# Kernel optimization log

Measured on AMD Instinct MI355X. Metric: run time of the kernel, lower is better.

## Reference

```python
import jax, jax.numpy as jnp
import numpy as np

V_IN = 32000
V_OUT = 32000
E = 1024
H = 1024
B = 16
T = 512


def _lstm_layer(xs, Wih, Whh, bih, bhh):
    # xs: [T, B, in_dim]; PyTorch gate order: i, f, g, o (each size H)
    gx = jnp.einsum('tbi,gi->tbg', xs, Wih) + bih + bhh  # [T, B, 4H]

    def step(carry, g_t):
        h, c = carry
        g = g_t + h @ Whh.T  # [B, 4H]
        i, f, gg, o = jnp.split(g, 4, axis=-1)
        i = jax.nn.sigmoid(i)
        f = jax.nn.sigmoid(f)
        gg = jnp.tanh(gg)
        o = jax.nn.sigmoid(o)
        c = f * c + i * gg
        h = o * jnp.tanh(c)
        return (h, c), h

    h0 = jnp.zeros((xs.shape[1], Whh.shape[1]), dtype=xs.dtype)
    c0 = jnp.zeros_like(h0)
    _, hs = jax.lax.scan(step, (h0, c0), gx)
    return hs  # [T, B, H]


def setup_inputs() -> dict:
    key = jax.random.key(0)
    ks = jax.random.split(key, 12)
    s_e = 1.0  # nn.Embedding default init is N(0,1)
    s_l = 1.0 / np.sqrt(H)  # LSTM/Linear uniform bound 1/sqrt(H)

    def u(k, shape):
        return jax.random.uniform(k, shape, jnp.float32, -s_l, s_l)

    return {
        'x': jax.random.randint(ks[0], (B, T), 0, V_IN),
        'emb': jax.random.normal(ks[1], (V_IN, E), jnp.float32) * s_e,
        'W_ih0': u(ks[2], (4 * H, E)),
        'W_hh0': u(ks[3], (4 * H, H)),
        'b_ih0': u(ks[4], (4 * H,)),
        'b_hh0': u(ks[5], (4 * H,)),
        'W_ih1': u(ks[6], (4 * H, H)),
        'W_hh1': u(ks[7], (4 * H, H)),
        'b_ih1': u(ks[8], (4 * H,)),
        'b_hh1': u(ks[9], (4 * H,)),
        'W_out': u(ks[10], (V_OUT, H)),
        'b_out': u(ks[11], (V_OUT,)),
    }


def reference(x, emb, W_ih0, W_hh0, b_ih0, b_hh0, W_ih1, W_hh1, b_ih1, b_hh1, W_out, b_out):
    # embedding + permute to [T, B, E]
    out = emb[x].transpose(1, 0, 2)
    out = _lstm_layer(out, W_ih0, W_hh0, b_ih0, b_hh0)
    out = _lstm_layer(out, W_ih1, W_hh1, b_ih1, b_hh1)
    logits = jnp.einsum('tbh,oh->tbo', out, W_out) + b_out
    return logits.transpose(1, 0, 2)  # [B, T, V_OUT]
```

## Files before the change

kernel.cpp:

```cpp
#include <hip/hip_runtime.h>
#include <cstdint>
#include <cstddef>

typedef __bf16 bf16;
typedef float f32x4 __attribute__((ext_vector_type(4)));
typedef bf16 bf16x8 __attribute__((ext_vector_type(8)));
typedef bf16 bf16x4 __attribute__((ext_vector_type(4)));

#define AS1 __attribute__((address_space(1)))
#define AS3 __attribute__((address_space(3)))

__device__ __forceinline__ void gload_lds16(const void* g, void* l) {
  __builtin_amdgcn_global_load_lds((AS1 void*)g, (AS3 void*)l, 16, 0, 0);
}

#define RING 8
#define FLAG_WORDS 1024

__global__ __launch_bounds__(256) void init_misc(
    const float* __restrict__ bih0, const float* __restrict__ bhh0,
    const float* __restrict__ bih1, const float* __restrict__ bhh1,
    float* __restrict__ bsum0, float* __restrict__ bsum1, unsigned* __restrict__ flags) {
  int i = blockIdx.x * 256 + threadIdx.x;
  if (i < 4096) {
    bsum0[i] = bih0[i] + bhh0[i];
    bsum1[i] = bih1[i] + bhh1[i];
  }
  if (i < FLAG_WORDS) flags[i] = 0u;
}

__global__ __launch_bounds__(256) void embed_gather(
    const int* __restrict__ x, const float* __restrict__ emb, bf16* __restrict__ xe, int T) {
  int row = blockIdx.x;
  int t = row >> 4, b = row & 15;
  int tok = x[b * T + t];
  int cix = threadIdx.x << 2;
  f32x4 v = *(const f32x4*)(emb + ((size_t)tok << 10) + cix);
  bf16x4 o;
  for (int j = 0; j < 4; ++j) o[j] = (bf16)v[j];
  *(bf16x4*)(xe + ((size_t)row << 10) + cix) = o;
}

template <int OUTMODE>
__global__ __launch_bounds__(256) void gemm_bf16(
    const bf16* __restrict__ A, const float* __restrict__ Bw,
    const float* __restrict__ bias, float* __restrict__ C,
    int M, int N, int K, int Tdim) {
  __shared__ bf16 aL[2][128 * 32];
  __shared__ bf16 bL[2][128 * 32];
  const int tid = threadIdx.x;
  const int l = tid & 63, w = tid >> 6;
  const int nbm = M >> 7;
  const int bm = blockIdx.x % nbm;
  const int bn = blockIdx.x / nbm;
  const int wr = (w >> 1) << 6, wc = (w & 1) << 6;
  const int NT = K >> 5;
  const int r16 = l & 15, kq = l >> 4;

  f32x4 acc[4][4];
  for (int m = 0; m < 4; ++m)
    for (int n = 0; n < 4; ++n) acc[m][n] = (f32x4){0.f, 0.f, 0.f, 0.f};

  for (int i = 0; i < 2; ++i) {
    int lin = tid + (i << 8);
    int r = lin >> 2, s = lin & 3, c = s ^ (r & 3);
    gload_lds16(A + (size_t)((bm << 7) + r) * K + (c << 3), &aL[0][lin << 3]);
  }
  for (int i = 0; i < 2; ++i) {
    int lin = tid + (i << 8);
    int r = lin >> 2, c = lin & 3;
    const float* src = Bw + (size_t)((bn << 7) + r) * K + (c << 3);
    f32x4 v0 = *(const f32x4*)src;
    f32x4 v1 = *(const f32x4*)(src + 4);
    bf16x8 o;
    for (int j = 0; j < 4; ++j) { o[j] = (bf16)v0[j]; o[j + 4] = (bf16)v1[j]; }
    *(bf16x8*)&bL[0][(r << 5) + ((c ^ (r & 3)) << 3)] = o;
  }
  __syncthreads();

  for (int kt = 0; kt < NT; ++kt) {
    const int cur = kt & 1;
    const bool pf = (kt + 1 < NT);
    f32x4 bv0[2], bv1[2];
    int br_[2], bs_[2];
    if (pf) {
      for (int i = 0; i < 2; ++i) {
        int lin = tid + (i << 8);
        int r = lin >> 2, s = lin & 3, c = s ^ (r & 3);
        gload_lds16(A + (size_t)((bm << 7) + r) * K + ((kt + 1) << 5) + (c << 3),
                    &aL[cur ^ 1][lin << 3]);
      }
      for (int i = 0; i < 2; ++i) {
        int lin = tid + (i << 8);
        int r = lin >> 2, c = lin & 3;
        const float* src = Bw + (size_t)((bn << 7) + r) * K + ((kt + 1) << 5) + (c << 3);
        bv0[i] = *(const f32x4*)src;
        bv1[i] = *(const f32x4*)(src + 4);
        br_[i] = r;
        bs_[i] = c ^ (r & 3);
      }
    }
    bf16x8 af[4], bfr[4];
    for (int m = 0; m < 4; ++m) {
      int row = wr + (m << 4) + r16;
      int ch = kq ^ (row & 3);
      af[m] = *(const bf16x8*)&aL[cur][(row << 5) + (ch << 3)];
    }
    for (int n = 0; n < 4; ++n) {
      int row = wc + (n << 4) + r16;
      int ch = kq ^ (row & 3);
      bfr[n] = *(const bf16x8*)&bL[cur][(row << 5) + (ch << 3)];
    }
    for (int m = 0; m < 4; ++m)
      for (int n = 0; n < 4; ++n)
        acc[m][n] = __builtin_amdgcn_mfma_f32_16x16x32_bf16(af[m], bfr[n], acc[m][n], 0, 0, 0);
    if (pf) {
      for (int i = 0; i < 2; ++i) {
        bf16x8 o;
        for (int j = 0; j < 4; ++j) { o[j] = (bf16)bv0[i][j]; o[j + 4] = (bf16)bv1[i][j]; }
        *(bf16x8*)&bL[cur ^ 1][(br_[i] << 5) + (bs_[i] << 3)] = o;
      }
    }
    __syncthreads();
  }

  float bvv[4];
  for (int n = 0; n < 4; ++n) bvv[n] = bias[(bn << 7) + wc + (n << 4) + r16];
  for (int m = 0; m < 4; ++m) {
    int Rbase = (bm << 7) + wr + (m << 4) + (kq << 2);
    for (int r = 0; r < 4; ++r) {
      int R = Rbase + r;
      size_t rowoff;
      if (OUTMODE == 0) {
        rowoff = (size_t)R * N;
      } else {
        int tt = R >> 4, bb = R & 15;
        rowoff = ((size_t)bb * Tdim + tt) * N;
      }
      for (int n = 0; n < 4; ++n)
        C[rowoff + (bn << 7) + wc + (n << 4) + r16] = acc[m][n][r] + bvv[n];
    }
  }
}

__global__ __launch_bounds__(256, 1) void lstm_pipe3(
    const float* __restrict__ gx,
    const float* __restrict__ Whh0,
    const float* __restrict__ Wih1,
    const float* __restrict__ Whh1,
    const float* __restrict__ bsum1,
    bf16* __restrict__ hs0t,
    bf16* __restrict__ hs1t,
    float* __restrict__ gx1,
    bf16* __restrict__ hs1rm,
    unsigned* __restrict__ flags,
    int T) {
  __shared__ bf16 wlds[4][16 * 1024];
  __shared__ unsigned short hb[4][64];
  __shared__ unsigned tokv[4];
  const int tid = threadIdx.x;
  const int l = tid & 63, w = tid >> 6;
  const int bid = blockIdx.x;
  const int r16 = l & 15, kq = l >> 4;
  unsigned* const fL0 = flags;
  unsigned* const fB = flags + 256;
  unsigned* const fL1 = flags + 512;
  const int typ = bid >> 6;
  const int lb = bid & 63;
  const int widx = lb * 4 + w;
  const int colbase = lb * 16 + w * 4;

  {
    const float* Wsrc = (typ == 0) ? Whh0 : ((typ == 1) ? Wih1 : Whh1);
    for (int it = 0; it < 32; ++it) {
      int lin = it * 64 + l;
      int row = lin >> 7, cs = lin & 127, c = cs ^ (row & 7);
      const float* s = Wsrc + (size_t)((row >> 2) * 1024 + colbase + (row & 3)) * 1024 + c * 8;
      f32x4 v0 = *(const f32x4*)s;
      f32x4 v1 = *(const f32x4*)(s + 4);
      bf16x8 o;
      for (int j = 0; j < 4; ++j) { o[j] = (bf16)v0[j]; o[j + 4] = (bf16)v1[j]; }
      *(bf16x8*)&wlds[w][row * 1024 + cs * 8] = o;
    }
  }
  if (tid < 4) tokv[tid] = 0;
  __syncthreads();

  const int gcol = (r16 >> 2) * 1024 + colbase + (r16 & 3);
  const int b0s = (r16 >> 2) & 1, b1s = (r16 >> 3) & 1;

  auto pollq = [&](unsigned* arr, unsigned tgt) {
    unsigned* q = arr + w * 64 + (l & 15) * 4;
    for (;;) {
      unsigned a0 = __hip_atomic_load(q + 0, __ATOMIC_RELAXED, __HIP_MEMORY_SCOPE_AGENT);
      unsigned a1 = __hip_atomic_load(q + 1, __ATOMIC_RELAXED, __HIP_MEMORY_SCOPE_AGENT);
      unsigned a2 = __hip_atomic_load(q + 2, __ATOMIC_RELAXED, __HIP_MEMORY_SCOPE_AGENT);
      unsigned a3 = __hip_atomic_load(q + 3, __ATOMIC_RELAXED, __HIP_MEMORY_SCOPE_AGENT);
      if (__all(a0 >= tgt && a1 >= tgt && a2 >= tgt && a3 >= tgt)) break;
      __builtin_amdgcn_s_sleep(2);
    }
    volatile unsigned* tk = tokv;
    if (l == 0) tk[w] = tgt;
    while (tk[0] < tgt || tk[1] < tgt || tk[2] < tgt || tk[3] < tgt) {
    }
    asm volatile("" ::: "memory");
  };
  auto poll1 = [&](unsigned* p, unsigned tgt) {
    while (__hip_atomic_load(p, __ATOMIC_RELAXED, __HIP_MEMORY_SCOPE_AGENT) < tgt)
      __builtin_amdgcn_s_sleep(2);
    asm volatile("" ::: "memory");
  };
  auto chain = [&](const bf16* plane) -> f32x4 {
    f32x4 acc = (f32x4){0.f, 0.f, 0.f, 0.f};
    const char* hp = (const char*)plane;
#pragma unroll 8
    for (int kk = 0; kk < 32; ++kk) {
      int tl = kk * 8 + kq * 2;
      unsigned long long lo = *(const unsigned long long*)(hp + tl * 128 + r16 * 8);
      unsigned long long hi = *(const unsigned long long*)(hp + tl * 128 + 128 + r16 * 8);
      union { struct { unsigned long long a, b; } u; bf16x8 v; } A;
      A.u.a = lo;
      A.u.b = hi;
      bf16x8 Bf = *(const bf16x8*)&wlds[w][r16 * 1024 + (((kk * 4 + kq) ^ (r16 & 7)) << 3)];
      acc = __builtin_amdgcn_mfma_f32_16x16x32_bf16(A.v, Bf, acc, 0, 0, 0);
    }
    return acc;
  };

  if (typ == 1) {
    const float bsv = bsum1[gcol];
    unsigned* const myflag = fB + widx;
    unsigned* const partner = fL1 + widx;
    for (int t = 0; t < T; ++t) {
      if (t >= RING) poll1(partner, (unsigned)(t - RING + 1));
      pollq(fL0, (unsigned)(t + 1));
      f32x4 acc = chain(hs0t + (size_t)t * 16384);
      for (int r = 0; r < 4; ++r) acc[r] += bsv;
      float* dst = gx1 + (size_t)(t & (RING - 1)) * 65536 + widx * 256 + r16 * 16 + kq * 4;
      asm volatile("global_store_dwordx4 %0, %1, off sc0 sc1" ::"v"(dst), "v"(acc) : "memory");
      asm volatile("s_waitcnt vmcnt(0)" ::: "memory");
      if (l == 0)
        __hip_atomic_store(myflag, (unsigned)(t + 1), __ATOMIC_RELAXED, __HIP_MEMORY_SCOPE_AGENT);
    }
    return;
  }

  float cst[4] = {0.f, 0.f, 0.f, 0.f};
  unsigned* const myflag = (typ == 0) ? (fL0 + widx) : (fL1 + widx);
  unsigned* const bpartner = fB + widx;
  bf16* const houts = (typ == 0) ? hs0t : hs1t;

  for (int t = 0; t < T; ++t) {
    float gxv[4];
    if (typ == 0) {
      for (int r = 0; r < 4; ++r)
        gxv[r] = gx[(size_t)(t * 16 + kq * 4 + r) * 4096 + gcol];
    }
    if (typ == 0) {
      if (t > 0) pollq(fL0, (unsigned)t);
    } else {
      poll1(bpartner, (unsigned)(t + 1));
      if (t > 0) pollq(fL1, (unsigned)t);
    }
    f32x4 acc = (f32x4){0.f, 0.f, 0.f, 0.f};
    if (t > 0) acc = chain(houts + (size_t)(t - 1) * 16384);
    if (typ == 0) {
      for (int r = 0; r < 4; ++r) acc[r] += gxv[r];
    } else {
      const float* gp = gx1 + (size_t)(t & (RING - 1)) * 65536 + widx * 256 + r16 * 16 + kq * 4;
      f32x4 g1;
      asm volatile("global_load_dwordx4 %0, %1, off sc0 sc1\ns_waitcnt vmcnt(0)"
                   : "=v"(g1) : "v"(gp) : "memory");
      for (int r = 0; r < 4; ++r) acc[r] += g1[r];
    }
    float hv[4];
    for (int r = 0; r < 4; ++r) {
      float own = acc[r];
      float p4 = __shfl_xor(own, 4, 64);
      float ev = b0s ? p4 : own;
      float ov = b0s ? own : p4;
      float ev8 = __shfl_xor(ev, 8, 64);
      float ov8 = __shfl_xor(ov, 8, 64);
      float xi = b1s ? ev8 : ev;
      float xf = b1s ? ov8 : ov;
      float xg = b1s ? ev : ev8;
      float xo = b1s ? ov : ov8;
      float ig = 1.f / (1.f + __expf(-xi));
      float fg = 1.f / (1.f + __expf(-xf));
      float eg = __expf(2.f * xg);
      float gv = 1.f - 2.f / (eg + 1.f);
      float og = 1.f / (1.f + __expf(-xo));
      cst[r] = fg * cst[r] + ig * gv;
      float ec = __expf(2.f * cst[r]);
      float th = 1.f - 2.f / (ec + 1.f);
      hv[r] = og * th;
    }
    if (r16 < 4) {
      volatile unsigned short* hbp = hb[w];
      for (int r = 0; r < 4; ++r) {
        bf16 hbv = (bf16)hv[r];
        hbp[(kq * 4 + r) * 4 + r16] = __builtin_bit_cast(unsigned short, hbv);
      }
    }
    unsigned long long rowv = 0;
    if (l < 16) rowv = *(volatile unsigned long long*)&hb[w][l * 4];
    if (l < 16) {
      char* dst = (char*)houts + (size_t)t * 32768 + widx * 128 + l * 8;
      asm volatile("global_store_dwordx2 %0, %1, off sc0 sc1" ::"v"(dst), "v"(rowv) : "memory");
    }
    asm volatile("s_waitcnt vmcnt(0)" ::: "memory");
    if (l == 0)
      __hip_atomic_store(myflag, (unsigned)(t + 1), __ATOMIC_RELAXED, __HIP_MEMORY_SCOPE_AGENT);
    if (typ == 1 + 1 && l < 16) {
      *(unsigned long long*)((char*)hs1rm + ((size_t)(t * 16 + l) * 1024 + colbase) * 2) = rowv;
    }
  }
}

extern "C" void kernel_launch(void* const* d_in, const int* in_sizes, int n_in,
                              void* d_out, int out_size, void* d_ws, size_t ws_size,
                              hipStream_t stream) {
  const int* x = (const int*)d_in[0];
  const float* emb = (const float*)d_in[1];
  const float* Wih0 = (const float*)d_in[2];
  const float* Whh0 = (const float*)d_in[3];
  const float* bih0 = (const float*)d_in[4];
  const float* bhh0 = (const float*)d_in[5];
  const float* Wih1 = (const float*)d_in[6];
  const float* Whh1 = (const float*)d_in[7];
  const float* bih1 = (const float*)d_in[8];
  const float* bhh1 = (const float*)d_in[9];
  const float* Wout = (const float*)d_in[10];
  const float* bout = (const float*)d_in[11];

  const int T = 512, H = 1024, V = 32000;
  const int M = T * 16;
  const size_t bfb = (size_t)M * H * 2;
  const size_t out_bytes = (size_t)out_size * 4;

  char* p = (char*)d_ws;
  bf16* hs1rm = (bf16*)p;         p += bfb;
  float* bsum0 = (float*)p;       p += 4096 * 4;
  float* bsum1 = (float*)p;       p += 4096 * 4;
  unsigned* flags = (unsigned*)p; p += FLAG_WORDS * 4;

  float* gx = (float*)d_out;
  float* gx1 = (float*)((char*)d_out + (512ull << 20));
  char* tail = (char*)d_out + out_bytes - 3 * bfb;
  bf16* xe = (bf16*)tail;
  bf16* hs0t = (bf16*)(tail + bfb);
  bf16* hs1t = (bf16*)(tail + 2 * bfb);

  init_misc<<<64, 256, 0, stream>>>(bih0, bhh0, bih1, bhh1, bsum0, bsum1, flags);
  embed_gather<<<M, 256, 0, stream>>>(x, emb, xe, T);
  gemm_bf16<0><<<(M / 128) * (4096 / 128), 256, 0, stream>>>(xe, Wih0, bsum0, gx, M, 4096, H, 0);
  lstm_pipe3<<<192, 256, 0, stream>>>(gx, Whh0, Wih1, Whh1, bsum1, hs0t, hs1t, gx1, hs1rm,
                                      flags, T);
  gemm_bf16<1><<<(M / 128) * (V / 128), 256, 0, stream>>>(hs1rm, Wout, bout, (float*)d_out,
                                                          M, V, H, T);
}
```

Baseline: 5.294 ms.

## Overlap output projection with LSTM recurrence in one persistent kernel

Merges the recurrent LSTM pipeline and the vocabulary projection GEMM into a single persistent kernel. It launches 64 extra blocks, and once the recurrent blocks finish they also pull output tiles from an atomic work queue, gated on per-row-chunk progress flags. This lets the large output GEMM run while the sequential recurrence is still going. The embedding gather is fused into the input-projection GEMM, and gx/hs/gx1 scratch buffers are placed inside not-yet-written regions of the output tensor in a new layout. The cost is more complex synchronization, and there is a risk that the scratch aliases get overwritten by output tiles before the recurrence has finished reading them.

Result: slower. 5.912 ms (+11.7%).

```diff
diff --git a/kernel.cpp b/kernel.cpp
--- a/kernel.cpp
+++ b/kernel.cpp
@@ -5,7 +5,6 @@
 typedef __bf16 bf16;
 typedef float f32x4 __attribute__((ext_vector_type(4)));
 typedef bf16 bf16x8 __attribute__((ext_vector_type(8)));
-typedef bf16 bf16x4 __attribute__((ext_vector_type(4)));
 
 #define AS1 __attribute__((address_space(1)))
 #define AS3 __attribute__((address_space(3)))
@@ -14,8 +13,13 @@
   __builtin_amdgcn_global_load_lds((AS1 void*)g, (AS3 void*)l, 16, 0, 0);
 }
 
-#define RING 8
 #define FLAG_WORDS 1024
+#define NTILE 16000u
+#define RW 32000ull
+
+__device__ __forceinline__ size_t LROW(int b, int t) {
+  return ((size_t)b * 512 + (size_t)t) * RW;
+}
 
 __global__ __launch_bounds__(256) void init_misc(
     const float* __restrict__ bih0, const float* __restrict__ bhh0,
@@ -29,77 +33,48 @@
   if (i < FLAG_WORDS) flags[i] = 0u;
 }
 
-__global__ __launch_bounds__(256) void embed_gather(
-    const int* __restrict__ x, const float* __restrict__ emb, bf16* __restrict__ xe, int T) {
-  int row = blockIdx.x;
-  int t = row >> 4, b = row & 15;
-  int tok = x[b * T + t];
-  int cix = threadIdx.x << 2;
-  f32x4 v = *(const f32x4*)(emb + ((size_t)tok << 10) + cix);
-  bf16x4 o;
-  for (int j = 0; j < 4; ++j) o[j] = (bf16)v[j];
-  *(bf16x4*)(xe + ((size_t)row << 10) + cix) = o;
-}
-
-template <int OUTMODE>
-__global__ __launch_bounds__(256) void gemm_bf16(
-    const bf16* __restrict__ A, const float* __restrict__ Bw,
-    const float* __restrict__ bias, float* __restrict__ C,
-    int M, int N, int K, int Tdim) {
-  __shared__ bf16 aL[2][128 * 32];
-  __shared__ bf16 bL[2][128 * 32];
+__global__ __launch_bounds__(256) void gemm_emb(
+    const int* __restrict__ x, const float* __restrict__ emb,
+    const float* __restrict__ Wih0, const float* __restrict__ bsum0,
+    float* __restrict__ C) {
+  __shared__ bf16 aL[2][4096];
+  __shared__ bf16 bL[2][4096];
   const int tid = threadIdx.x;
   const int l = tid & 63, w = tid >> 6;
-  const int nbm = M >> 7;
-  const int bm = blockIdx.x % nbm;
-  const int bn = blockIdx.x / nbm;
+  const int bm = blockIdx.x & 63;
+  const int bn = blockIdx.x >> 6;
   const int wr = (w >> 1) << 6, wc = (w & 1) << 6;
-  const int NT = K >> 5;
   const int r16 = l & 15, kq = l >> 4;
 
   f32x4 acc[4][4];
   for (int m = 0; m < 4; ++m)
     for (int n = 0; n < 4; ++n) acc[m][n] = (f32x4){0.f, 0.f, 0.f, 0.f};
 
-  for (int i = 0; i < 2; ++i) {
-    int lin = tid + (i << 8);
-    int r = lin >> 2, s = lin & 3, c = s ^ (r & 3);
-    gload_lds16(A + (size_t)((bm << 7) + r) * K + (c << 3), &aL[0][lin << 3]);
-  }
-  for (int i = 0; i < 2; ++i) {
-    int lin = tid + (i << 8);
-    int r = lin >> 2, c = lin & 3;
-    const float* src = Bw + (size_t)((bn << 7) + r) * K + (c << 3);
-    f32x4 v0 = *(const f32x4*)src;
-    f32x4 v1 = *(const f32x4*)(src + 4);
-    bf16x8 o;
-    for (int j = 0; j < 4; ++j) { o[j] = (bf16)v0[j]; o[j + 4] = (bf16)v1[j]; }
-    *(bf16x8*)&bL[0][(r << 5) + ((c ^ (r & 3)) << 3)] = o;
-  }
+  auto stage = [&](int kt, int buf) {
+    for (int i = 0; i < 2; ++i) {
+      int lin = tid + (i << 8);
+      int r = lin >> 2, c = lin & 3;
+      int rg = (bm << 7) + r;
+      int tok = x[((rg & 15) << 9) + (rg >> 4)];
+      const float* sa = emb + ((size_t)tok << 10) + (kt << 5) + (c << 3);
+      f32x4 a0 = *(const f32x4*)sa;
+      f32x4 a1 = *(const f32x4*)(sa + 4);
+      bf16x8 oa;
+      for (int j = 0; j < 4; ++j) { oa[j] = (bf16)a0[j]; oa[j + 4] = (bf16)a1[j]; }
+      *(bf16x8*)&aL[buf][(r << 5) + ((c ^ (r & 3)) << 3)] = oa;
+      const float* sb = Wih0 + (size_t)((bn << 7) + r) * 1024 + (kt << 5) + (c << 3);
+      f32x4 b0 = *(const f32x4*)sb;
+      f32x4 b1 = *(const f32x4*)(sb + 4);
+      bf16x8 ob;
+      for (int j = 0; j < 4; ++j) { ob[j] = (bf16)b0[j]; ob[j + 4] = (bf16)b1[j]; }
+      *(bf16x8*)&bL[buf][(r << 5) + ((c ^ (r & 3)) << 3)] = ob;
+    }
+  };
+  stage(0, 0);
   __syncthreads();
-
-  for (int kt = 0; kt < NT; ++kt) {
-    const int cur = kt & 1;
-    const bool pf = (kt + 1 < NT);
-    f32x4 bv0[2], bv1[2];
-    int br_[2], bs_[2];
-    if (pf) {
-      for (int i = 0; i < 2; ++i) {
-        int lin = tid + (i << 8);
-        int r = lin >> 2, s = lin & 3, c = s ^ (r & 3);
-        gload_lds16(A + (size_t)((bm << 7) + r) * K + ((kt + 1) << 5) + (c << 3),
-                    &aL[cur ^ 1][lin << 3]);
-      }
-      for (int i = 0; i < 2; ++i) {
-        int lin = tid + (i << 8);
-        int r = lin >> 2, c = lin & 3;
-        const float* src = Bw + (size_t)((bn << 7) + r) * K + ((kt + 1) << 5) + (c << 3);
-        bv0[i] = *(const f32x4*)src;
-        bv1[i] = *(const f32x4*)(src + 4);
-        br_[i] = r;
-        bs_[i] = c ^ (r & 3);
-      }
-    }
+  for (int kt = 0; kt < 32; ++kt) {
+    int cur = kt & 1;
+    if (kt + 1 < 32) stage(kt + 1, cur ^ 1);
     bf16x8 af[4], bfr[4];
     for (int m = 0; m < 4; ++m) {
       int row = wr + (m << 4) + r16;
@@ -114,63 +89,46 @@
     for (int m = 0; m < 4; ++m)
       for (int n = 0; n < 4; ++n)
         acc[m][n] = __builtin_amdgcn_mfma_f32_16x16x32_bf16(af[m], bfr[n], acc[m][n], 0, 0, 0);
-    if (pf) {
-      for (int i = 0; i < 2; ++i) {
-        bf16x8 o;
-        for (int j = 0; j < 4; ++j) { o[j] = (bf16)bv0[i][j]; o[j + 4] = (bf16)bv1[i][j]; }
-        *(bf16x8*)&bL[cur ^ 1][(br_[i] << 5) + (bs_[i] << 3)] = o;
-      }
-    }
     __syncthreads();
   }
-
   float bvv[4];
-  for (int n = 0; n < 4; ++n) bvv[n] = bias[(bn << 7) + wc + (n << 4) + r16];
+  for (int n = 0; n < 4; ++n) bvv[n] = bsum0[(bn << 7) + wc + (n << 4) + r16];
   for (int m = 0; m < 4; ++m) {
     int Rbase = (bm << 7) + wr + (m << 4) + (kq << 2);
     for (int r = 0; r < 4; ++r) {
       int R = Rbase + r;
-      size_t rowoff;
-      if (OUTMODE == 0) {
-        rowoff = (size_t)R * N;
-      } else {
-        int tt = R >> 4, bb = R & 15;
-        rowoff = ((size_t)bb * Tdim + tt) * N;
-      }
+      int tt = R >> 4, bb = R & 15;
+      size_t rowoff = LROW(bb, tt);
       for (int n = 0; n < 4; ++n)
         C[rowoff + (bn << 7) + wc + (n << 4) + r16] = acc[m][n][r] + bvv[n];
     }
   }
 }
 
-__global__ __launch_bounds__(256, 1) void lstm_pipe3(
-    const float* __restrict__ gx,
-    const float* __restrict__ Whh0,
-    const float* __restrict__ Wih1,
-    const float* __restrict__ Whh1,
-    const float* __restrict__ bsum1,
-    bf16* __restrict__ hs0t,
-    bf16* __restrict__ hs1t,
-    float* __restrict__ gx1,
-    bf16* __restrict__ hs1rm,
-    unsigned* __restrict__ flags,
-    int T) {
+__global__ __launch_bounds__(256, 1) void lstm_mega(
+    const float* __restrict__ Whh0, const float* __restrict__ Wih1,
+    const float* __restrict__ Whh1, const float* __restrict__ bsum1,
+    bf16* __restrict__ hs1rm, const float* __restrict__ Wout,
+    const float* __restrict__ bout, float* __restrict__ C,
+    unsigned* __restrict__ flags) {
   __shared__ bf16 wlds[4][16 * 1024];
   __shared__ unsigned short hb[4][64];
-  __shared__ unsigned tokv[4];
-  const int tid = threadIdx.x;
-  const int l = tid & 63, w = tid >> 6;
+  __shared__ unsigned tokv[3][4];
+  __shared__ unsigned qsh;
+  const int tid = threadIdx.x, l = tid & 63, w = tid >> 6;
   const int bid = blockIdx.x;
   const int r16 = l & 15, kq = l >> 4;
   unsigned* const fL0 = flags;
   unsigned* const fB = flags + 256;
   unsigned* const fL1 = flags + 512;
+  unsigned* const qctr = flags + 768;
   const int typ = bid >> 6;
   const int lb = bid & 63;
   const int widx = lb * 4 + w;
   const int colbase = lb * 16 + w * 4;
-
-  {
+  const int T = 512;
+
+  if (typ < 3) {
     const float* Wsrc = (typ == 0) ? Whh0 : ((typ == 1) ? Wih1 : Whh1);
     for (int it = 0; it < 32; ++it) {
       int lin = it * 64 + l;
@@ -183,13 +141,10 @@
       *(bf16x8*)&wlds[w][row * 1024 + cs * 8] = o;
     }
   }
-  if (tid < 4) tokv[tid] = 0;
+  if (tid < 12) ((unsigned*)tokv)[tid] = 0;
   __syncthreads();
 
-  const int gcol = (r16 >> 2) * 1024 + colbase + (r16 & 3);
-  const int b0s = (r16 >> 2) & 1, b1s = (r16 >> 3) & 1;
-
-  auto pollq = [&](unsigned* arr, unsigned tgt) {
+  auto pollq = [&](int gid, unsigned* arr, unsigned tgt) {
     unsigned* q = arr + w * 64 + (l & 15) * 4;
     for (;;) {
       unsigned a0 = __hip_atomic_load(q + 0, __ATOMIC_RELAXED, __HIP_MEMORY_SCOPE_AGENT);
@@ -199,8 +154,8 @@
       if (__all(a0 >= tgt && a1 >= tgt && a2 >= tgt && a3 >= tgt)) break;
       __builtin_amdgcn_s_sleep(2);
     }
-    volatile unsigned* tk = tokv;
-    if (l == 0) tk[w] = tgt;
+    volatile unsigned* tk = tokv[gid];
+    if (l == 0 && tk[w] < tgt) tk[w] = tgt;
     while (tk[0] < tgt || tk[1] < tgt || tk[2] < tgt || tk[3] < tgt) {
     }
     asm volatile("" ::: "memory");
@@ -226,54 +181,17 @@
     }
     return acc;
   };
-
-  if (typ == 1) {
-    const float bsv = bsum1[gcol];
-    unsigned* const myflag = fB + widx;
-    unsigned* const partner = fL1 + widx;
-    for (int t = 0; t < T; ++t) {
-      if (t >= RING) poll1(partner, (unsigned)(t - RING + 1));
-      pollq(fL0, (unsigned)(t + 1));
-      f32x4 acc = chain(hs0t + (size_t)t * 16384);
-      for (int r = 0; r < 4; ++r) acc[r] += bsv;
-      float* dst = gx1 + (size_t)(t & (RING - 1)) * 65536 + widx * 256 + r16 * 16 + kq * 4;
-      asm volatile("global_store_dwordx4 %0, %1, off sc0 sc1" ::"v"(dst), "v"(acc) : "memory");
-      asm volatile("s_waitcnt vmcnt(0)" ::: "memory");
-      if (l == 0)
-        __hip_atomic_store(myflag, (unsigned)(t + 1), __ATOMIC_RELAXED, __HIP_MEMORY_SCOPE_AGENT);
-    }
-    return;
-  }
-
-  float cst[4] = {0.f, 0.f, 0.f, 0.f};
-  unsigned* const myflag = (typ == 0) ? (fL0 + widx) : (fL1 + widx);
-  unsigned* const bpartner = fB + widx;
-  bf16* const houts = (typ == 0) ? hs0t : hs1t;
-
-  for (int t = 0; t < T; ++t) {
-    float gxv[4];
-    if (typ == 0) {
-      for (int r = 0; r < 4; ++r)
-        gxv[r] = gx[(size_t)(t * 16 + kq * 4 + r) * 4096 + gcol];
-    }
-    if (typ == 0) {
-      if (t > 0) pollq(fL0, (unsigned)t);
-    } else {
-      poll1(bpartner, (unsigned)(t + 1));
-      if (t > 0) pollq(fL1, (unsigned)t);
-    }
-    f32x4 acc = (f32x4){0.f, 0.f, 0.f, 0.f};
-    if (t > 0) acc = chain(houts + (size_t)(t - 1) * 16384);
-    if (typ == 0) {
-      for (int r = 0; r < 4; ++r) acc[r] += gxv[r];
-    } else {
-      const float* gp = gx1 + (size_t)(t & (RING - 1)) * 65536 + widx * 256 + r16 * 16 + kq * 4;
-      f32x4 g1;
-      asm volatile("global_load_dwordx4 %0, %1, off sc0 sc1\ns_waitcnt vmcnt(0)"
-                   : "=v"(g1) : "v"(gp) : "memory");
-      for (int r = 0; r < 4; ++r) acc[r] += g1[r];
-    }
-    float hv[4];
+  auto hs0p = [&](int t) { return (bf16*)(C + LROW(0, t) + 4096); };
+  auto hs1p = [&](int t) { return (bf16*)(C + LROW(0, t) + 12288); };
+  auto gx1p = [&](int t, unsigned idx) -> float* {
+    if (idx < 27904u) return C + LROW(1, t) + 4096 + idx;
+    if (idx < 55808u) return C + LROW(2, t) + 4096 + (idx - 27904u);
+    return C + LROW(3, t) + 4096 + (idx - 55808u);
+  };
+  const int gcol = (r16 >> 2) * 1024 + colbase + (r16 & 3);
+  const int b0s = (r16 >> 2) & 1, b1s = (r16 >> 3) & 1;
+
+  auto gates = [&](f32x4 acc, float* cst, float* hv) {
     for (int r = 0; r < 4; ++r) {
       float own = acc[r];
       float p4 = __shfl_xor(own, 4, 64);
@@ -295,6 +213,8 @@
       float th = 1.f - 2.f / (ec + 1.f);
       hv[r] = og * th;
     }
+  };
+  auto transpose_store = [&](float* hv, char* dstbase) -> unsigned long long {
     if (r16 < 4) {
       volatile unsigned short* hbp = hb[w];
       for (int r = 0; r < 4; ++r) {
@@ -303,16 +223,161 @@
       }
     }
     unsigned long long rowv = 0;
-    if (l < 16) rowv = *(volatile unsigned long long*)&hb[w][l * 4];
     if (l < 16) {
-      char* dst = (char*)houts + (size_t)t * 32768 + widx * 128 + l * 8;
+      rowv = *(volatile unsigned long long*)&hb[w][l * 4];
+      char* dst = dstbase + widx * 128 + l * 8;
       asm volatile("global_store_dwordx2 %0, %1, off sc0 sc1" ::"v"(dst), "v"(rowv) : "memory");
     }
-    asm volatile("s_waitcnt vmcnt(0)" ::: "memory");
-    if (l == 0)
-      __hip_atomic_store(myflag, (unsigned)(t + 1), __ATOMIC_RELAXED, __HIP_MEMORY_SCOPE_AGENT);
-    if (typ == 1 + 1 && l < 16) {
-      *(unsigned long long*)((char*)hs1rm + ((size_t)(t * 16 + l) * 1024 + colbase) * 2) = rowv;
+    return rowv;
+  };
+
+  if (typ == 0) {
+    float cst[4] = {0.f, 0.f, 0.f, 0.f};
+    unsigned* const myflag = fL0 + widx;
+    for (int t = 0; t < T; ++t) {
+      float gxv[4];
+      for (int r = 0; r < 4; ++r) gxv[r] = C[LROW(kq * 4 + r, t) + gcol];
+      if (t > 0) pollq(0, fL0, (unsigned)t);
+      f32x4 acc = (f32x4){0.f, 0.f, 0.f, 0.f};
+      if (t > 0) acc = chain(hs0p(t - 1));
+      for (int r = 0; r < 4; ++r) acc[r] += gxv[r];
+      float hv[4];
+      gates(acc, cst, hv);
+      transpose_store(hv, (char*)hs0p(t));
+      asm volatile("s_waitcnt vmcnt(0)" ::: "memory");
+      if (l == 0)
+        __hip_atomic_store(myflag, (unsigned)(t + 1), __ATOMIC_RELAXED, __HIP_MEMORY_SCOPE_AGENT);
+    }
+  } else if (typ == 1) {
+    const float bsv = bsum1[gcol];
+    unsigned* const myflag = fB + widx;
+    for (int t = 0; t < T; ++t) {
+      pollq(0, fL0, (unsigned)(t + 1));
+      f32x4 acc = chain(hs0p(t));
+      for (int r = 0; r < 4; ++r) acc[r] += bsv;
+      float* dst = gx1p(t, (unsigned)(widx * 256 + r16 * 16 + kq * 4));
+      asm volatile("global_store_dwordx4 %0, %1, off sc0 sc1" ::"v"(dst), "v"(acc) : "memory");
+      asm volatile("s_waitcnt vmcnt(0)" ::: "memory");
+      if (l == 0)
+        __hip_atomic_store(myflag, (unsigned)(t + 1), __ATOMIC_RELAXED, __HIP_MEMORY_SCOPE_AGENT);
+    }
+  } else if (typ == 2) {
+    float cst[4] = {0.f, 0.f, 0.f, 0.f};
+    unsigned* const myflag = fL1 + widx;
+    unsigned* const bpartner = fB + widx;
+    for (int t = 0; t < T; ++t) {
+      poll1(bpartner, (unsigned)(t + 1));
+      if (t > 0) pollq(2, fL1, (unsigned)t);
+      f32x4 acc = (f32x4){0.f, 0.f, 0.f, 0.f};
+      if (t > 0) acc = chain(hs1p(t - 1));
+      const float* gp = gx1p(t, (unsigned)(widx * 256 + r16 * 16 + kq * 4));
+      f32x4 g1;
+      asm volatile("global_load_dwordx4 %0, %1, off sc0 sc1\ns_waitcnt vmcnt(0)"
+                   : "=v"(g1) : "v"(gp) : "memory");
+      for (int r = 0; r < 4; ++r) acc[r] += g1[r];
+      float hv[4];
+      gates(acc, cst, hv);
+      unsigned long long rowv = transpose_store(hv, (char*)hs1p(t));
+      if (l < 16) {
+        char* dst = (char*)hs1rm + ((size_t)(t * 16 + l) * 1024 + colbase) * 2;
+        asm volatile("global_store_dwordx2 %0, %1, off sc0 sc1" ::"v"(dst), "v"(rowv) : "memory");
+      }
+      asm volatile("s_waitcnt vmcnt(0)" ::: "memory");
+      if (l == 0)
+        __hip_atomic_store(myflag, (unsigned)(t + 1), __ATOMIC_RELAXED, __HIP_MEMORY_SCOPE_AGENT);
+    }
+  }
+
+  bf16* const paL = &wlds[0][0];
+  bf16* const pbL = &wlds[0][8192];
+  const int wr = (w >> 1) << 6, wc2 = (w & 1) << 6;
+  for (;;) {
+    __syncthreads();
+    if (tid == 0) qsh = atomicAdd(qctr, 1u);
+    __syncthreads();
+    unsigned tau = qsh;
+    if (tau >= NTILE) break;
+    int rc = (int)(tau / 250u), cc = (int)(tau - (unsigned)rc * 250u);
+    unsigned g0 = (unsigned)(8 * rc + 9);
+    if (g0 > 512u) g0 = 512u;
+    pollq(0, fL0, g0);
+    pollq(2, fL1, g0);
+    __syncthreads();
+    f32x4 acc[4][4];
+    for (int m = 0; m < 4; ++m)
+      for (int n = 0; n < 4; ++n) acc[m][n] = (f32x4){0.f, 0.f, 0.f, 0.f};
+    for (int i = 0; i < 2; ++i) {
+      int lin = tid + (i << 8);
+      int r = lin >> 2, s2 = lin & 3, c = s2 ^ (r & 3);
+      gload_lds16(hs1rm + (size_t)(rc * 128 + r) * 1024 + (c << 3), &paL[lin << 3]);
+    }
+    for (int i = 0; i < 2; ++i) {
+      int lin = tid + (i << 8);
+      int r = lin >> 2, c = lin & 3;
+      const float* src = Wout + (size_t)(cc * 128 + r) * 1024 + (c << 3);
+      f32x4 v0 = *(const f32x4*)src;
+      f32x4 v1 = *(const f32x4*)(src + 4);
+      bf16x8 o;
+      for (int j = 0; j < 4; ++j) { o[j] = (bf16)v0[j]; o[j + 4] = (bf16)v1[j]; }
+      *(bf16x8*)&pbL[(r << 5) + ((c ^ (r & 3)) << 3)] = o;
+    }
+    __syncthreads();
+    for (int kt = 0; kt < 32; ++kt) {
+      const int cur = kt & 1;
+      const bool pf = (kt + 1 < 32);
+      f32x4 bv0[2], bv1[2];
+      int br_[2], bs_[2];
+      if (pf) {
+        for (int i = 0; i < 2; ++i) {
+          int lin = tid + (i << 8);
+          int r = lin >> 2, s2 = lin & 3, c = s2 ^ (r & 3);
+          gload_lds16(hs1rm + (size_t)(rc * 128 + r) * 1024 + ((kt + 1) << 5) + (c << 3),
+                      &paL[(cur ^ 1) * 4096 + (lin << 3)]);
+        }
+        for (int i = 0; i < 2; ++i) {
+          int lin = tid + (i << 8);
+          int r = lin >> 2, c = lin & 3;
+          const float* src = Wout + (size_t)(cc * 128 + r) * 1024 + ((kt + 1) << 5) + (c << 3);
+          bv0[i] = *(const f32x4*)src;
+          bv1[i] = *(const f32x4*)(src + 4);
+          br_[i] = r;
+          bs_[i] = c ^ (r & 3);
+        }
+      }
+      bf16x8 af[4], bfr[4];
+      for (int m = 0; m < 4; ++m) {
+        int row = wr + (m << 4) + r16;
+        int ch = kq ^ (row & 3);
+        af[m] = *(const bf16x8*)&paL[cur * 4096 + (row << 5) + (ch << 3)];
+      }
+      for (int n = 0; n < 4; ++n) {
+        int row = wc2 + (n << 4) + r16;
+        int ch = kq ^ (row & 3);
+        bfr[n] = *(const bf16x8*)&pbL[cur * 4096 + (row << 5) + (ch << 3)];
+      }
+      for (int m = 0; m < 4; ++m)
+        for (int n = 0; n < 4; ++n)
+          acc[m][n] = __builtin_amdgcn_mfma_f32_16x16x32_bf16(af[m], bfr[n], acc[m][n], 0, 0, 0);
+      if (pf) {
+        for (int i = 0; i < 2; ++i) {
+          bf16x8 o;
+          for (int j = 0; j < 4; ++j) { o[j] = (bf16)bv0[i][j]; o[j + 4] = (bf16)bv1[i][j]; }
+          *(bf16x8*)&pbL[(cur ^ 1) * 4096 + (br_[i] << 5) + (bs_[i] << 3)] = o;
+        }
+      }
+      __syncthreads();
+    }
+    float bvv[4];
+    for (int n = 0; n < 4; ++n) bvv[n] = bout[cc * 128 + wc2 + (n << 4) + r16];
+    for (int m = 0; m < 4; ++m) {
+      int Rbase = rc * 128 + wr + (m << 4) + (kq << 2);
+      for (int r = 0; r < 4; ++r) {
+        int R = Rbase + r;
+        int tt = R >> 4, bb = R & 15;
+        size_t rowoff = LROW(bb, tt);
+        for (int n = 0; n < 4; ++n)
+          C[rowoff + cc * 128 + wc2 + (n << 4) + r16] = acc[m][n][r] + bvv[n];
+      }
     }
   }
 }
@@ -333,29 +398,19 @@
   const float* Wout = (const float*)d_in[10];
   const float* bout = (const float*)d_in[11];
 
-  const int T = 512, H = 1024, V = 32000;
-  const int M = T * 16;
-  const size_t bfb = (size_t)M * H * 2;
-  const size_t out_bytes = (size_t)out_size * 4;
+  const int M = 8192;
+  const size_t bfb = (size_t)M * 1024 * 2;
 
   char* p = (char*)d_ws;
   bf16* hs1rm = (bf16*)p;         p += bfb;
   float* bsum0 = (float*)p;       p += 4096 * 4;
   float* bsum1 = (float*)p;       p += 4096 * 4;
   unsigned* flags = (unsigned*)p; p += FLAG_WORDS * 4;
-
-  float* gx = (float*)d_out;
-  float* gx1 = (float*)((char*)d_out + (512ull << 20));
-  char* tail = (char*)d_out + out_bytes - 3 * bfb;
-  bf16* xe = (bf16*)tail;
-  bf16* hs0t = (bf16*)(tail + bfb);
-  bf16* hs1t = (bf16*)(tail + 2 * bfb);
+  (void)ws_size;
+
+  float* C = (float*)d_out;
 
   init_misc<<<64, 256, 0, stream>>>(bih0, bhh0, bih1, bhh1, bsum0, bsum1, flags);
-  embed_gather<<<M, 256, 0, stream>>>(x, emb, xe, T);
-  gemm_bf16<0><<<(M / 128) * (4096 / 128), 256, 0, stream>>>(xe, Wih0, bsum0, gx, M, 4096, H, 0);
-  lstm_pipe3<<<192, 256, 0, stream>>>(gx, Whh0, Wih1, Whh1, bsum1, hs0t, hs1t, gx1, hs1rm,
-                                      flags, T);
-  gemm_bf16<1><<<(M / 128) * (V / 128), 256, 0, stream>>>(hs1rm, Wout, bout, (float*)d_out,
-                                                          M, V, H, T);
-}
+  gemm_emb<<<64 * 32, 256, 0, stream>>>(x, emb, Wih0, bsum0, C);
+  lstm_mega<<<256, 256, 0, stream>>>(Whh0, Wih1, Whh1, bsum1, hs1rm, Wout, bout, C, flags);
+}
```
